# Kernel optimization log

Hardware: AMD Instinct MI355X
Metric: run time of the kernel (lower is better)

## Reference

```python
import jax, jax.numpy as jnp
import numpy as np

KH = KW = 3
STRIDE = 1
PAD = 1
DIL = 1


def _bilinear_gather(data, py, px):
    # data: [B,C,H,W]; py,px: [B,KK,Ho,Wo] absolute sample coords
    B, C, H, W = data.shape
    y0 = jnp.floor(py)
    x0 = jnp.floor(px)
    wy1 = py - y0  # frac weights
    wx1 = px - x0
    wy0 = 1.0 - wy1
    wx0 = 1.0 - wx1
    flat = data.reshape(B, C, H * W)

    def gather(yi, xi):
        valid = (yi >= 0) & (yi < H) & (xi >= 0) & (xi < W)
        yc = jnp.clip(yi, 0, H - 1).astype(jnp.int32)
        xc = jnp.clip(xi, 0, W - 1).astype(jnp.int32)
        idx = yc * W + xc  # [B,KK,Ho,Wo]
        vals = jax.vmap(lambda im, ix: im[:, ix])(flat, idx)  # [B,C,KK,Ho,Wo]
        return vals * valid[:, None].astype(data.dtype)

    out = (gather(y0, x0) * (wy0 * wx0)[:, None]
           + gather(y0, x0 + 1) * (wy0 * wx1)[:, None]
           + gather(y0 + 1, x0) * (wy1 * wx0)[:, None]
           + gather(y0 + 1, x0 + 1) * (wy1 * wx1)[:, None])
    return out  # [B,C,KK,Ho,Wo]


def setup_inputs() -> dict:
    key = jax.random.key(0)
    k1, k2, k3 = jax.random.split(key, 3)
    data = jax.random.normal(k1, (8, 64, 128, 128), dtype=jnp.float32)
    offset = jax.random.normal(k2, (8, 18, 128, 128), dtype=jnp.float32)
    n = 64 * KH * KW
    stdv = 1.0 / np.sqrt(n)
    weight = jax.random.uniform(k3, (64, 64, KH, KW), dtype=jnp.float32,
                                minval=-stdv, maxval=stdv)
    return {"data": data, "offset": offset, "weight": weight}


def reference(data, offset, weight):
    B, C, H, W = data.shape
    Ho = (H + 2 * PAD - (DIL * (KH - 1) + 1)) // STRIDE + 1
    Wo = (W + 2 * PAD - (DIL * (KW - 1) + 1)) // STRIDE + 1
    KK = KH * KW
    # offset layout (deformable_groups=1): [B, 2*KK, Ho, Wo], interleaved (dy, dx) per kernel pt
    off = offset.reshape(B, KK, 2, Ho, Wo)
    off_y = off[:, :, 0]  # [B,KK,Ho,Wo]
    off_x = off[:, :, 1]
    ki = (jnp.arange(KK) // KW).astype(data.dtype)  # kernel row
    kj = (jnp.arange(KK) % KW).astype(data.dtype)   # kernel col
    base_y = (jnp.arange(Ho, dtype=data.dtype) * STRIDE - PAD)[None, :, None] \
             + (ki * DIL)[:, None, None]            # [KK,Ho,1]
    base_x = (jnp.arange(Wo, dtype=data.dtype) * STRIDE - PAD)[None, None, :] \
             + (kj * DIL)[:, None, None]            # [KK,1,Wo]
    py = off_y + base_y[None]  # [B,KK,Ho,Wo]
    px = off_x + base_x[None]
    sampled = _bilinear_gather(data, py, px)  # [B,C,KK,Ho,Wo]
    O = weight.shape[0]
    out = jnp.einsum('bckhw,ock->bohw', sampled, weight.reshape(O, C, KK))
    return out
```

## Files before the change

kernel.cpp:

```cpp
#include <hip/hip_runtime.h>

#define HH 128
#define WW 128
#define CC 64
#define OO 64
#define KK 9
#define PLANE (HH * WW)

#define BAND 8
#define BAND_B (BAND * 128 * 64)

typedef _Float16 half8v __attribute__((ext_vector_type(8)));
typedef _Float16 half2v __attribute__((ext_vector_type(2)));
typedef float floatx4 __attribute__((ext_vector_type(4)));

__device__ __forceinline__ unsigned pkpair(float a, float b) {
    return __builtin_bit_cast(unsigned, __builtin_amdgcn_cvt_pkrtz(a, b));
}
__device__ __forceinline__ half2v h2(unsigned u) {
    return __builtin_bit_cast(half2v, u);
}

__global__ __launch_bounds__(256)
void prep_kernel(const float* __restrict__ in, const float* __restrict__ wsrc,
                 unsigned short* __restrict__ outT, _Float16* __restrict__ wt4) {
    __shared__ unsigned tile[64 * 36];
    int blk = blockIdx.x;
    int t = threadIdx.x;
    if (blk < 2048) {
        int b = blk & 7;
        int rest = blk >> 3;
        int y = rest >> 1;
        int xh = rest & 1;
        int p = t & 63;
        int cg = t >> 6;
        const float* src = in + (size_t)(b * 64) * PLANE + y * WW + xh * 64 + p;
#pragma unroll
        for (int i = 0; i < 8; ++i) {
            int c0 = cg * 16 + 2 * i;
            float v0 = src[(size_t)c0 * PLANE];
            float v1 = src[(size_t)(c0 + 1) * PLANE];
            unsigned lo = __builtin_bit_cast(unsigned short, (_Float16)v0);
            unsigned hi = __builtin_bit_cast(unsigned short, (_Float16)v1);
            tile[p * 36 + (c0 >> 1)] = lo | (hi << 16);
        }
        __syncthreads();
        int p2 = t >> 2;
        int q = t & 3;
        const unsigned* s = &tile[p2 * 36 + q * 8];
        uint4 w0 = *(const uint4*)s;
        uint4 w1 = *(const uint4*)(s + 4);
        int half = q >> 1;
        char* dst = (char*)outT + ((size_t)(b * 2 + half) << 20)
                  + (size_t)(y * 128 + xh * 64 + p2) * 64 + (q & 1) * 32;
        *(uint4*)dst = w0;
        *(uint4*)(dst + 16) = w1;
    } else {
        int idx = (blk - 2048) * 256 + t;
        if (idx < 2 * KK * 4 * 64 * 8) {
            int j = idx & 7;
            int lane = (idx >> 3) & 63;
            int nt = (idx >> 9) & 3;
            int pk = idx >> 11;
            int k = pk % 9;
            int pass = pk / 9;
            int o = nt * 16 + (lane & 15);
            int c = pass * 32 + (lane >> 4) * 8 + j;
            wt4[idx] = (_Float16)wsrc[(o * 64 + c) * 9 + k];
        }
    }
}

__global__ __launch_bounds__(256, 2)
void deform_mfma_kernel(const unsigned short* __restrict__ dataT,
                        const float* __restrict__ offset,
                        const _Float16* __restrict__ wt4,
                        float* __restrict__ out) {
    __shared__ __align__(16) char SB[BAND_B];
    __shared__ unsigned sOff[KK][128];
    __shared__ uint2 sWt[KK][128];

    const int t = threadIdx.x;
    const int lane = t & 63;
    const int w = t >> 6;
    const int quad = lane >> 4;
    const int l15 = lane & 15;
    const int raw = blockIdx.x;
    const int b = raw & 7;
    const int ho = raw >> 3;
    const int mbase = w * 32;
    const int bs = min(max(ho - 3, 0), HH - BAND);

#pragma unroll
    for (int i = 0; i < 5; ++i) {
        int idx = i * 64 + lane;
        if (idx < 288) {
            int k = idx >> 5;
            int px = mbase + (idx & 31);
            const float* offp = offset + ((size_t)(b * 18) + 2 * k) * PLANE + ho * WW + px;
            float oy = offp[0];
            float ox = offp[PLANE];
            float py = (float)(ho - 1 + k / 3) + oy;
            float pxx = (float)(px - 1 + k % 3) + ox;
            float y0f = floorf(py);
            float x0f = floorf(pxx);
            float fy = py - y0f;
            float fx = pxx - x0f;
            int y0 = (int)y0f, x0 = (int)x0f;
            int y1 = y0 + 1, x1 = x0 + 1;
            float wy0 = (1.f - fy) * ((y0 >= 0 && y0 < HH) ? 1.f : 0.f);
            float wy1 = fy * ((y1 >= 0 && y1 < HH) ? 1.f : 0.f);
            float wx0 = (1.f - fx) * ((x0 >= 0 && x0 < WW) ? 1.f : 0.f);
            float wx1 = fx * ((x1 >= 0 && x1 < WW) ? 1.f : 0.f);
            int yc0 = min(max(y0, 0), HH - 1);
            int yc1 = min(max(y1, 0), HH - 1);
            int x_lo = min(max(x0, 0), WW - 2);
            float wA = ((x0 == x_lo) ? wx0 : 0.f) + ((x1 == x_lo) ? wx1 : 0.f);
            float wB = ((x0 == x_lo + 1) ? wx0 : 0.f) + ((x1 == x_lo + 1) ? wx1 : 0.f);

            unsigned v0, v1, d;
            {
                int r = yc0 - bs;
                if (wy0 == 0.f) { v0 = (unsigned)x_lo; d = 0; }
                else if ((unsigned)r < BAND) { v0 = (unsigned)(r * 128 + x_lo); d = 0; }
                else { v0 = (unsigned)(yc0 * 128 + x_lo); d = 0x4000u; }
            }
            {
                int r = yc1 - bs;
                if (wy1 == 0.f) v1 = (unsigned)x_lo;
                else if ((unsigned)r < BAND) v1 = (unsigned)(r * 128 + x_lo);
                else { v1 = (unsigned)(yc1 * 128 + x_lo); d |= 0x20000000u; }
            }
            sOff[k][px] = d | v0 | (v1 << 15);
            sWt[k][px] = make_uint2(pkpair(wy0 * wA, wy0 * wB),
                                    pkpair(wy1 * wA, wy1 * wB));
        }
    }

    floatx4 acc[2][4];
#pragma unroll
    for (int mt = 0; mt < 2; ++mt)
#pragma unroll
        for (int nt = 0; nt < 4; ++nt)
            acc[mt][nt] = (floatx4){0.f, 0.f, 0.f, 0.f};

    const int p0 = mbase + l15;
    const int p1 = mbase + 16 + l15;

    for (int pass = 0; pass < 2; ++pass) {
        if (pass) __syncthreads();
        const char* gh = (const char*)dataT + ((size_t)(b * 2 + pass) << 20);
        {
            const char* gsrc = gh + (unsigned)(bs * 8192);
#pragma unroll
            for (int i = 0; i < 16; ++i) {
                int u = i * 256 + t;
                uint4 v = *(const uint4*)(gsrc + (size_t)u * 16);
                int pxl = u >> 2, q = u & 3;
                *(uint4*)(SB + pxl * 64 + (((q + pxl) & 3) << 4)) = v;
            }
        }
        __syncthreads();

        auto compute = [&](unsigned d, uint2 wp, floatx4* accrow) {
            unsigned v0 = d & 0x3fffu;
            unsigned v1 = (d >> 15) & 0x3fffu;
            unsigned rot00 = ((quad + v0) & 3u) << 4;
            unsigned rot01 = ((quad + v0 + 1) & 3u) << 4;
            unsigned rot10 = ((quad + v1) & 3u) << 4;
            unsigned rot11 = ((quad + v1 + 1) & 3u) << 4;
            uint4 v00 = *(const uint4*)(SB + ((v0 & 1023u) << 6) + rot00);
            uint4 v01 = *(const uint4*)(SB + ((v0 & 1023u) << 6) + 64 + rot01);
            uint4 v10 = *(const uint4*)(SB + ((v1 & 1023u) << 6) + rot10);
            uint4 v11 = *(const uint4*)(SB + ((v1 & 1023u) << 6) + 64 + rot11);
            if (d & 0x4000u) {
                const char* g = gh + ((size_t)v0 << 6) + (quad << 4);
                v00 = *(const uint4*)g;
                v01 = *(const uint4*)(g + 64);
            }
            if (d & 0x20000000u) {
                const char* g = gh + ((size_t)v1 << 6) + (quad << 4);
                v10 = *(const uint4*)g;
                v11 = *(const uint4*)(g + 64);
            }
            half2v wv0 = h2(wp.x), wv1 = h2(wp.y);
            half2v h00 = __builtin_shufflevector(wv0, wv0, 0, 0);
            half2v h01 = __builtin_shufflevector(wv0, wv0, 1, 1);
            half2v h10 = __builtin_shufflevector(wv1, wv1, 0, 0);
            half2v h11 = __builtin_shufflevector(wv1, wv1, 1, 1);
            half2v s0 = h2(v00.x) * h00 + h2(v01.x) * h01 + h2(v10.x) * h10 + h2(v11.x) * h11;
            half2v s1 = h2(v00.y) * h00 + h2(v01.y) * h01 + h2(v10.y) * h10 + h2(v11.y) * h11;
            half2v s2 = h2(v00.z) * h00 + h2(v01.z) * h01 + h2(v10.z) * h10 + h2(v11.z) * h11;
            half2v s3 = h2(v00.w) * h00 + h2(v01.w) * h01 + h2(v10.w) * h10 + h2(v11.w) * h11;
            uint4 sv = make_uint4(__builtin_bit_cast(unsigned, s0),
                                  __builtin_bit_cast(unsigned, s1),
                                  __builtin_bit_cast(unsigned, s2),
                                  __builtin_bit_cast(unsigned, s3));
            half8v afrag = __builtin_bit_cast(half8v, sv);
#pragma unroll
            for (int nt = 0; nt < 4; ++nt)
                accrow[nt] = __builtin_amdgcn_mfma_f32_16x16x32_f16(
                    afrag, __builtin_bit_cast(half8v, ((const uint4*)nullptr == nullptr, accrow[nt])), accrow[nt], 0, 0, 0);
        };
        (void)compute;

        unsigned dc0 = sOff[0][p0], dc1 = sOff[0][p1];
        uint2 wc0 = sWt[0][p0], wc1 = sWt[0][p1];
        uint4 bc[4];
        {
            const uint4* wk = (const uint4*)wt4 + (size_t)(pass * 9 * 4) * 64 + lane;
#pragma unroll
            for (int nt = 0; nt < 4; ++nt) bc[nt] = wk[nt * 64];
        }
        for (int k = 0; k < KK; ++k) {
            unsigned dn0 = 0, dn1 = 0;
            uint2 wn0 = make_uint2(0, 0), wn1 = make_uint2(0, 0);
            uint4 bn[4];
            if (k < 8) {
                dn0 = sOff[k + 1][p0];
                dn1 = sOff[k + 1][p1];
                wn0 = sWt[k + 1][p0];
                wn1 = sWt[k + 1][p1];
                const uint4* wk = (const uint4*)wt4 + (size_t)((pass * 9 + k + 1) * 4) * 64 + lane;
#pragma unroll
                for (int nt = 0; nt < 4; ++nt) bn[nt] = wk[nt * 64];
            }
#pragma unroll
            for (int mt = 0; mt < 2; ++mt) {
                unsigned d = mt ? dc1 : dc0;
                uint2 wp = mt ? wc1 : wc0;
                unsigned v0 = d & 0x3fffu;
                unsigned v1 = (d >> 15) & 0x3fffu;
                unsigned rot00 = ((quad + v0) & 3u) << 4;
                unsigned rot01 = ((quad + v0 + 1) & 3u) << 4;
                unsigned rot10 = ((quad + v1) & 3u) << 4;
                unsigned rot11 = ((quad + v1 + 1) & 3u) << 4;
                uint4 v00 = *(const uint4*)(SB + ((v0 & 1023u) << 6) + rot00);
                uint4 v01 = *(const uint4*)(SB + ((v0 & 1023u) << 6) + 64 + rot01);
                uint4 v10 = *(const uint4*)(SB + ((v1 & 1023u) << 6) + rot10);
                uint4 v11 = *(const uint4*)(SB + ((v1 & 1023u) << 6) + 64 + rot11);
                if (d & 0x4000u) {
                    const char* g = gh + ((size_t)v0 << 6) + (quad << 4);
                    v00 = *(const uint4*)g;
                    v01 = *(const uint4*)(g + 64);
                }
                if (d & 0x20000000u) {
                    const char* g = gh + ((size_t)v1 << 6) + (quad << 4);
                    v10 = *(const uint4*)g;
                    v11 = *(const uint4*)(g + 64);
                }
                half2v wv0 = h2(wp.x), wv1 = h2(wp.y);
                half2v h00 = __builtin_shufflevector(wv0, wv0, 0, 0);
                half2v h01 = __builtin_shufflevector(wv0, wv0, 1, 1);
                half2v h10 = __builtin_shufflevector(wv1, wv1, 0, 0);
                half2v h11 = __builtin_shufflevector(wv1, wv1, 1, 1);
                half2v s0 = h2(v00.x) * h00 + h2(v01.x) * h01 + h2(v10.x) * h10 + h2(v11.x) * h11;
                half2v s1 = h2(v00.y) * h00 + h2(v01.y) * h01 + h2(v10.y) * h10 + h2(v11.y) * h11;
                half2v s2 = h2(v00.z) * h00 + h2(v01.z) * h01 + h2(v10.z) * h10 + h2(v11.z) * h11;
                half2v s3 = h2(v00.w) * h00 + h2(v01.w) * h01 + h2(v10.w) * h10 + h2(v11.w) * h11;
                uint4 sv = make_uint4(__builtin_bit_cast(unsigned, s0),
                                      __builtin_bit_cast(unsigned, s1),
                                      __builtin_bit_cast(unsigned, s2),
                                      __builtin_bit_cast(unsigned, s3));
                half8v afrag = __builtin_bit_cast(half8v, sv);
#pragma unroll
                for (int nt = 0; nt < 4; ++nt)
                    acc[mt][nt] = __builtin_amdgcn_mfma_f32_16x16x32_f16(
                        afrag, __builtin_bit_cast(half8v, bc[nt]), acc[mt][nt], 0, 0, 0);
            }
            if (k < 8) {
                dc0 = dn0; dc1 = dn1; wc0 = wn0; wc1 = wn1;
#pragma unroll
                for (int nt = 0; nt < 4; ++nt) bc[nt] = bn[nt];
            }
        }
    }

#pragma unroll
    for (int mt = 0; mt < 2; ++mt)
#pragma unroll
        for (int nt = 0; nt < 4; ++nt) {
            int o = nt * 16 + l15;
            int px = mbase + mt * 16 + quad * 4;
            float* dst = out + (size_t)(b * 64 + o) * PLANE + ho * 128 + px;
            *(floatx4*)dst = acc[mt][nt];
        }
}

__global__ void transpose_weight_kernel(const float* __restrict__ w,
                                        float* __restrict__ wt) {
    int i = blockIdx.x * 256 + threadIdx.x;
    if (i < CC * KK * OO) {
        int o = i & 63;
        int ck = i >> 6;
        wt[i] = w[o * (CC * KK) + ck];
    }
}

__global__ __launch_bounds__(256)
void deform_conv_kernel(const float* __restrict__ data,
                        const float* __restrict__ offset,
                        const float* __restrict__ wt,
                        float* __restrict__ out) {
    const int tid = threadIdx.x;
    const int wo = tid & 127;
    int ohalf = tid >> 7;
    ohalf = __builtin_amdgcn_readfirstlane(ohalf);
    const int row = blockIdx.x;
    const int b = row >> 7;
    const int ho = row & 127;
    int abyte[KK][4];
    float wgt[KK][4];
    const float* offBase = offset + ((size_t)b * 18) * PLANE + ho * WW + wo;
#pragma unroll
    for (int k = 0; k < KK; ++k) {
        float oy = offBase[(2 * k) * PLANE];
        float ox = offBase[(2 * k + 1) * PLANE];
        float py = oy + (float)(ho - 1 + k / 3);
        float px = ox + (float)(wo - 1 + k % 3);
        float y0f = floorf(py);
        float x0f = floorf(px);
        float wy1 = py - y0f, wx1 = px - x0f;
        float wy0 = 1.f - wy1, wx0 = 1.f - wx1;
        int y0 = (int)y0f, x0 = (int)x0f;
        int y1 = y0 + 1, x1 = x0 + 1;
        float my0 = (y0 >= 0 && y0 < HH) ? 1.f : 0.f;
        float my1 = (y1 >= 0 && y1 < HH) ? 1.f : 0.f;
        float mx0 = (x0 >= 0 && x0 < WW) ? 1.f : 0.f;
        float mx1 = (x1 >= 0 && x1 < WW) ? 1.f : 0.f;
        int yc0 = min(max(y0, 0), HH - 1);
        int yc1 = min(max(y1, 0), HH - 1);
        int xc0 = min(max(x0, 0), WW - 1);
        int xc1 = min(max(x1, 0), WW - 1);
        abyte[k][0] = (yc0 * WW + xc0) * 4;
        abyte[k][1] = (yc0 * WW + xc1) * 4;
        abyte[k][2] = (yc1 * WW + xc0) * 4;
        abyte[k][3] = (yc1 * WW + xc1) * 4;
        wgt[k][0] = wy0 * wx0 * my0 * mx0;
        wgt[k][1] = wy0 * wx1 * my0 * mx1;
        wgt[k][2] = wy1 * wx0 * my1 * mx0;
        wgt[k][3] = wy1 * wx1 * my1 * mx1;
    }
    float acc[32];
#pragma unroll
    for (int j = 0; j < 32; ++j) acc[j] = 0.f;
    const float* planeBase = data + (size_t)b * CC * PLANE;
    const float4* wt4base = (const float4*)wt + ohalf * 8;
    for (int c = 0; c < CC; ++c) {
        const char* pc = (const char*)(planeBase + c * PLANE);
#pragma unroll
        for (int k = 0; k < KK; ++k) {
            float v00 = *(const float*)(pc + abyte[k][0]);
            float v01 = *(const float*)(pc + abyte[k][1]);
            float v10 = *(const float*)(pc + abyte[k][2]);
            float v11 = *(const float*)(pc + abyte[k][3]);
            float s = wgt[k][0] * v00 + wgt[k][1] * v01 +
                      wgt[k][2] * v10 + wgt[k][3] * v11;
            const float4* wp = wt4base + (c * KK + k) * 16;
#pragma unroll
            for (int j = 0; j < 8; ++j) {
                float4 wv = wp[j];
                acc[4 * j + 0] += s * wv.x;
                acc[4 * j + 1] += s * wv.y;
                acc[4 * j + 2] += s * wv.z;
                acc[4 * j + 3] += s * wv.w;
            }
        }
    }
    float* outp = out + ((size_t)b * OO + ohalf * 32) * PLANE + ho * WW + wo;
#pragma unroll
    for (int j = 0; j < 32; ++j) outp[j * PLANE] = acc[j];
}

extern "C" void kernel_launch(void* const* d_in, const int* in_sizes, int n_in,
                              void* d_out, int out_size, void* d_ws, size_t ws_size,
                              hipStream_t stream) {
    const float* data = (const float*)d_in[0];
    const float* offset = (const float*)d_in[1];
    const float* weight = (const float*)d_in[2];
    float* out = (float*)d_out;

    const size_t DATA_T_BYTES = (size_t)8 * 2 * 128 * 128 * 64;
    const size_t WT4_BYTES = (size_t)2 * KK * 4 * 64 * 8 * 2;

    if (ws_size >= DATA_T_BYTES + WT4_BYTES) {
        unsigned short* dataT = (unsigned short*)d_ws;
        _Float16* wt4 = (_Float16*)((char*)d_ws + DATA_T_BYTES);
        prep_kernel<<<2048 + 144, 256, 0, stream>>>(data, weight, dataT, wt4);
        deform_mfma_kernel<<<8 * HH, 256, 0, stream>>>(dataT, offset, wt4, out);
    } else {
        float* wt = (float*)d_ws;
        int nw = CC * KK * OO;
        transpose_weight_kernel<<<(nw + 255) / 256, 256, 0, stream>>>(weight, wt);
        deform_conv_kernel<<<8 * HH, 256, 0, stream>>>(data, offset, wt, out);
    }
}
```

Measured before the change: 134.8 us.

## Read bottom bilinear row from global, drop LDS swizzle, repad prep tile

The main kernel now always fetches the second (y1) bilinear row directly from global memory and issues those loads at the start of each kernel-point iteration so their latency overlaps other work. Only the y0 row is still read from the LDS band, and the LDS rotation swizzle is removed so band fills and reads use plain linear addressing. The prep kernel pads its transpose tile to a stride of 37 words and remaps threads for the store phase to reduce LDS bank conflicts. The trade-off is more global and L2 traffic plus possible LDS bank conflicts from the unswizzled layout. The 37-word padding also makes the 128-bit LDS reads unaligned.

```diff
diff --git a/kernel.cpp b/kernel.cpp
--- a/kernel.cpp
+++ b/kernel.cpp
@@ -24,7 +24,7 @@
 __global__ __launch_bounds__(256)
 void prep_kernel(const float* __restrict__ in, const float* __restrict__ wsrc,
                  unsigned short* __restrict__ outT, _Float16* __restrict__ wt4) {
-    __shared__ unsigned tile[64 * 36];
+    __shared__ unsigned tile[64 * 37];
     int blk = blockIdx.x;
     int t = threadIdx.x;
     if (blk < 2048) {
@@ -42,17 +42,18 @@
             float v1 = src[(size_t)(c0 + 1) * PLANE];
             unsigned lo = __builtin_bit_cast(unsigned short, (_Float16)v0);
             unsigned hi = __builtin_bit_cast(unsigned short, (_Float16)v1);
-            tile[p * 36 + (c0 >> 1)] = lo | (hi << 16);
+            tile[p * 37 + (c0 >> 1)] = lo | (hi << 16);
         }
         __syncthreads();
-        int p2 = t >> 2;
-        int q = t & 3;
-        const unsigned* s = &tile[p2 * 36 + q * 8];
+        int h = t >> 7;
+        int r = t & 127;
+        int px = r >> 1;
+        int sub = r & 1;
+        const unsigned* s = &tile[px * 37 + h * 16 + sub * 8];
         uint4 w0 = *(const uint4*)s;
         uint4 w1 = *(const uint4*)(s + 4);
-        int half = q >> 1;
-        char* dst = (char*)outT + ((size_t)(b * 2 + half) << 20)
-                  + (size_t)(y * 128 + xh * 64 + p2) * 64 + (q & 1) * 32;
+        char* dst = (char*)outT + ((size_t)(b * 2 + h) << 20)
+                  + (size_t)(y * 128 + xh * 64 + px) * 64 + sub * 32;
         *(uint4*)dst = w0;
         *(uint4*)(dst + 16) = w1;
     } else {
@@ -118,20 +119,15 @@
             float wA = ((x0 == x_lo) ? wx0 : 0.f) + ((x1 == x_lo) ? wx1 : 0.f);
             float wB = ((x0 == x_lo + 1) ? wx0 : 0.f) + ((x1 == x_lo + 1) ? wx1 : 0.f);
 
-            unsigned v0, v1, d;
+            unsigned v0, fb = 0;
             {
                 int r = yc0 - bs;
-                if (wy0 == 0.f) { v0 = (unsigned)x_lo; d = 0; }
-                else if ((unsigned)r < BAND) { v0 = (unsigned)(r * 128 + x_lo); d = 0; }
-                else { v0 = (unsigned)(yc0 * 128 + x_lo); d = 0x4000u; }
-            }
-            {
-                int r = yc1 - bs;
-                if (wy1 == 0.f) v1 = (unsigned)x_lo;
-                else if ((unsigned)r < BAND) v1 = (unsigned)(r * 128 + x_lo);
-                else { v1 = (unsigned)(yc1 * 128 + x_lo); d |= 0x20000000u; }
-            }
-            sOff[k][px] = d | v0 | (v1 << 15);
+                if (wy0 == 0.f) v0 = (unsigned)x_lo;
+                else if ((unsigned)r < BAND) v0 = (unsigned)(r * 128 + x_lo);
+                else { v0 = (unsigned)(yc0 * 128 + x_lo); fb = 0x4000u; }
+            }
+            unsigned v1 = (unsigned)(yc1 * 128 + x_lo);
+            sOff[k][px] = v0 | fb | (v1 << 15);
             sWt[k][px] = make_uint2(pkpair(wy0 * wA, wy0 * wB),
                                     pkpair(wy1 * wA, wy1 * wB));
         }
@@ -146,6 +142,7 @@
 
     const int p0 = mbase + l15;
     const int p1 = mbase + 16 + l15;
+    const unsigned qoff = (unsigned)(quad * 16);
 
     for (int pass = 0; pass < 2; ++pass) {
         if (pass) __syncthreads();
@@ -156,56 +153,13 @@
             for (int i = 0; i < 16; ++i) {
                 int u = i * 256 + t;
                 uint4 v = *(const uint4*)(gsrc + (size_t)u * 16);
-                int pxl = u >> 2, q = u & 3;
-                *(uint4*)(SB + pxl * 64 + (((q + pxl) & 3) << 4)) = v;
+                *(uint4*)(SB + u * 16) = v;
             }
         }
         __syncthreads();
 
-        auto compute = [&](unsigned d, uint2 wp, floatx4* accrow) {
-            unsigned v0 = d & 0x3fffu;
-            unsigned v1 = (d >> 15) & 0x3fffu;
-            unsigned rot00 = ((quad + v0) & 3u) << 4;
-            unsigned rot01 = ((quad + v0 + 1) & 3u) << 4;
-            unsigned rot10 = ((quad + v1) & 3u) << 4;
-            unsigned rot11 = ((quad + v1 + 1) & 3u) << 4;
-            uint4 v00 = *(const uint4*)(SB + ((v0 & 1023u) << 6) + rot00);
-            uint4 v01 = *(const uint4*)(SB + ((v0 & 1023u) << 6) + 64 + rot01);
-            uint4 v10 = *(const uint4*)(SB + ((v1 & 1023u) << 6) + rot10);
-            uint4 v11 = *(const uint4*)(SB + ((v1 & 1023u) << 6) + 64 + rot11);
-            if (d & 0x4000u) {
-                const char* g = gh + ((size_t)v0 << 6) + (quad << 4);
-                v00 = *(const uint4*)g;
-                v01 = *(const uint4*)(g + 64);
-            }
-            if (d & 0x20000000u) {
-                const char* g = gh + ((size_t)v1 << 6) + (quad << 4);
-                v10 = *(const uint4*)g;
-                v11 = *(const uint4*)(g + 64);
-            }
-            half2v wv0 = h2(wp.x), wv1 = h2(wp.y);
-            half2v h00 = __builtin_shufflevector(wv0, wv0, 0, 0);
-            half2v h01 = __builtin_shufflevector(wv0, wv0, 1, 1);
-            half2v h10 = __builtin_shufflevector(wv1, wv1, 0, 0);
-            half2v h11 = __builtin_shufflevector(wv1, wv1, 1, 1);
-            half2v s0 = h2(v00.x) * h00 + h2(v01.x) * h01 + h2(v10.x) * h10 + h2(v11.x) * h11;
-            half2v s1 = h2(v00.y) * h00 + h2(v01.y) * h01 + h2(v10.y) * h10 + h2(v11.y) * h11;
-            half2v s2 = h2(v00.z) * h00 + h2(v01.z) * h01 + h2(v10.z) * h10 + h2(v11.z) * h11;
-            half2v s3 = h2(v00.w) * h00 + h2(v01.w) * h01 + h2(v10.w) * h10 + h2(v11.w) * h11;
-            uint4 sv = make_uint4(__builtin_bit_cast(unsigned, s0),
-                                  __builtin_bit_cast(unsigned, s1),
-                                  __builtin_bit_cast(unsigned, s2),
-                                  __builtin_bit_cast(unsigned, s3));
-            half8v afrag = __builtin_bit_cast(half8v, sv);
-#pragma unroll
-            for (int nt = 0; nt < 4; ++nt)
-                accrow[nt] = __builtin_amdgcn_mfma_f32_16x16x32_f16(
-                    afrag, __builtin_bit_cast(half8v, ((const uint4*)nullptr == nullptr, accrow[nt])), accrow[nt], 0, 0, 0);
-        };
-        (void)compute;
-
-        unsigned dc0 = sOff[0][p0], dc1 = sOff[0][p1];
-        uint2 wc0 = sWt[0][p0], wc1 = sWt[0][p1];
+        unsigned dc[2] = { sOff[0][p0], sOff[0][p1] };
+        uint2 wc[2] = { sWt[0][p0], sWt[0][p1] };
         uint4 bc[4];
         {
             const uint4* wk = (const uint4*)wt4 + (size_t)(pass * 9 * 4) * 64 + lane;
@@ -213,51 +167,46 @@
             for (int nt = 0; nt < 4; ++nt) bc[nt] = wk[nt * 64];
         }
         for (int k = 0; k < KK; ++k) {
-            unsigned dn0 = 0, dn1 = 0;
-            uint2 wn0 = make_uint2(0, 0), wn1 = make_uint2(0, 0);
+            uint4 y1a[2], y1b[2];
+#pragma unroll
+            for (int mt = 0; mt < 2; ++mt) {
+                const char* g = gh + ((size_t)(dc[mt] >> 15) << 6) + qoff;
+                y1a[mt] = *(const uint4*)g;
+                y1b[mt] = *(const uint4*)(g + 64);
+            }
+            unsigned dn[2] = {0, 0};
+            uint2 wn[2] = {make_uint2(0, 0), make_uint2(0, 0)};
             uint4 bn[4];
             if (k < 8) {
-                dn0 = sOff[k + 1][p0];
-                dn1 = sOff[k + 1][p1];
-                wn0 = sWt[k + 1][p0];
-                wn1 = sWt[k + 1][p1];
+                dn[0] = sOff[k + 1][p0];
+                dn[1] = sOff[k + 1][p1];
+                wn[0] = sWt[k + 1][p0];
+                wn[1] = sWt[k + 1][p1];
                 const uint4* wk = (const uint4*)wt4 + (size_t)((pass * 9 + k + 1) * 4) * 64 + lane;
 #pragma unroll
                 for (int nt = 0; nt < 4; ++nt) bn[nt] = wk[nt * 64];
             }
 #pragma unroll
             for (int mt = 0; mt < 2; ++mt) {
-                unsigned d = mt ? dc1 : dc0;
-                uint2 wp = mt ? wc1 : wc0;
+                unsigned d = dc[mt];
                 unsigned v0 = d & 0x3fffu;
-                unsigned v1 = (d >> 15) & 0x3fffu;
-                unsigned rot00 = ((quad + v0) & 3u) << 4;
-                unsigned rot01 = ((quad + v0 + 1) & 3u) << 4;
-                unsigned rot10 = ((quad + v1) & 3u) << 4;
-                unsigned rot11 = ((quad + v1 + 1) & 3u) << 4;
-                uint4 v00 = *(const uint4*)(SB + ((v0 & 1023u) << 6) + rot00);
-                uint4 v01 = *(const uint4*)(SB + ((v0 & 1023u) << 6) + 64 + rot01);
-                uint4 v10 = *(const uint4*)(SB + ((v1 & 1023u) << 6) + rot10);
-                uint4 v11 = *(const uint4*)(SB + ((v1 & 1023u) << 6) + 64 + rot11);
+                uint4 a0 = *(const uint4*)(SB + ((v0 & 1023u) << 6) + qoff);
+                uint4 a1 = *(const uint4*)(SB + ((v0 & 1023u) << 6) + 64 + qoff);
                 if (d & 0x4000u) {
-                    const char* g = gh + ((size_t)v0 << 6) + (quad << 4);
-                    v00 = *(const uint4*)g;
-                    v01 = *(const uint4*)(g + 64);
+                    const char* g = gh + ((size_t)v0 << 6) + qoff;
+                    a0 = *(const uint4*)g;
+                    a1 = *(const uint4*)(g + 64);
                 }
-                if (d & 0x20000000u) {
-                    const char* g = gh + ((size_t)v1 << 6) + (quad << 4);
-                    v10 = *(const uint4*)g;
-                    v11 = *(const uint4*)(g + 64);
-                }
-                half2v wv0 = h2(wp.x), wv1 = h2(wp.y);
+                half2v wv0 = h2(wc[mt].x), wv1 = h2(wc[mt].y);
                 half2v h00 = __builtin_shufflevector(wv0, wv0, 0, 0);
                 half2v h01 = __builtin_shufflevector(wv0, wv0, 1, 1);
                 half2v h10 = __builtin_shufflevector(wv1, wv1, 0, 0);
                 half2v h11 = __builtin_shufflevector(wv1, wv1, 1, 1);
-                half2v s0 = h2(v00.x) * h00 + h2(v01.x) * h01 + h2(v10.x) * h10 + h2(v11.x) * h11;
-                half2v s1 = h2(v00.y) * h00 + h2(v01.y) * h01 + h2(v10.y) * h10 + h2(v11.y) * h11;
-                half2v s2 = h2(v00.z) * h00 + h2(v01.z) * h01 + h2(v10.z) * h10 + h2(v11.z) * h11;
-                half2v s3 = h2(v00.w) * h00 + h2(v01.w) * h01 + h2(v10.w) * h10 + h2(v11.w) * h11;
+                uint4 c0 = y1a[mt], c1 = y1b[mt];
+                half2v s0 = h2(a0.x) * h00 + h2(a1.x) * h01 + h2(c0.x) * h10 + h2(c1.x) * h11;
+                half2v s1 = h2(a0.y) * h00 + h2(a1.y) * h01 + h2(c0.y) * h10 + h2(c1.y) * h11;
+                half2v s2 = h2(a0.z) * h00 + h2(a1.z) * h01 + h2(c0.z) * h10 + h2(c1.z) * h11;
+                half2v s3 = h2(a0.w) * h00 + h2(a1.w) * h01 + h2(c0.w) * h10 + h2(c1.w) * h11;
                 uint4 sv = make_uint4(__builtin_bit_cast(unsigned, s0),
                                       __builtin_bit_cast(unsigned, s1),
                                       __builtin_bit_cast(unsigned, s2),
@@ -269,7 +218,8 @@
                         afrag, __builtin_bit_cast(half8v, bc[nt]), acc[mt][nt], 0, 0, 0);
             }
             if (k < 8) {
-                dc0 = dn0; dc1 = dn1; wc0 = wn0; wc1 = wn1;
+                dc[0] = dn[0]; dc[1] = dn[1];
+                wc[0] = wn[0]; wc[1] = wn[1];
 #pragma unroll
                 for (int nt = 0; nt < 4; ++nt) bc[nt] = bn[nt];
             }
```

Measured after the change: 143.9 us. 6.7% more time.
